# Performance work log

Hardware: AMD Instinct MI355X
Metric: run time of the kernel (lower is better)

Reference implementation:

```python
import jax, jax.numpy as jnp
import numpy as np

T, B, L, F, H = 32, 32, 128, 512, 1024
SCALE = 1.0 / np.sqrt(float(L))  # 1/sqrt(max_demonstration_length)


def _lstm_step(h, c, x, W_ih, W_hh, b_ih, b_hh):
    # PyTorch LSTM gate order: i, f, g, o
    gates = x @ W_ih.T + b_ih + h @ W_hh.T + b_hh
    i, f, g, o = jnp.split(gates, 4, axis=-1)
    c = jax.nn.sigmoid(f) * c + jax.nn.sigmoid(i) * jnp.tanh(g)
    h = jax.nn.sigmoid(o) * jnp.tanh(c)
    return h, c


def setup_inputs() -> dict:
    key = jax.random.key(0)
    ks = jax.random.split(key, 20)
    s = 0.02
    d = {
        'demonstration': jax.random.normal(ks[0], (T, B, L, F), jnp.float32),
        'demonstration_lengths': jax.random.randint(ks[1], (B,), 0, L),
        'current_obs': jax.random.normal(ks[2], (T, B, F), jnp.float32),
        'h0': jnp.zeros((1, B, H), jnp.float32),
        'c0': jnp.zeros((1, B, H), jnp.float32),
        # demonstration_encoder LSTM(F -> H)
        'enc_W_ih': jax.random.normal(ks[3], (4 * H, F), jnp.float32) * s,
        'enc_W_hh': jax.random.normal(ks[4], (4 * H, H), jnp.float32) * s,
        'enc_b_ih': jnp.zeros((4 * H,), jnp.float32),
        'enc_b_hh': jnp.zeros((4 * H,), jnp.float32),
        # attn Linear(H -> H)
        'attn_W': jax.random.normal(ks[5], (H, H), jnp.float32) * s,
        'attn_b': jnp.zeros((H,), jnp.float32),
        # attn_combine MLP: (F + H) -> 4H -> H
        'mlp_W1': jax.random.normal(ks[6], (4 * H, F + H), jnp.float32) * s,
        'mlp_b1': jnp.zeros((4 * H,), jnp.float32),
        'mlp_W2': jax.random.normal(ks[7], (H, 4 * H), jnp.float32) * s,
        'mlp_b2': jnp.zeros((H,), jnp.float32),
        # recurrent LSTM(H -> H)
        'lstm_W_ih': jax.random.normal(ks[8], (4 * H, H), jnp.float32) * s,
        'lstm_W_hh': jax.random.normal(ks[9], (4 * H, H), jnp.float32) * s,
        'lstm_b_ih': jnp.zeros((4 * H,), jnp.float32),
        'lstm_b_hh': jnp.zeros((4 * H,), jnp.float32),
    }
    return d


def reference(demonstration, demonstration_lengths, current_obs, h0, c0,
              enc_W_ih, enc_W_hh, enc_b_ih, enc_b_hh,
              attn_W, attn_b, mlp_W1, mlp_b1, mlp_W2, mlp_b2,
              lstm_W_ih, lstm_W_hh, lstm_b_ih, lstm_b_hh):
    # Encode demonstration[0] (B, L, F) with an LSTM over the L axis.
    x_demo = jnp.transpose(demonstration[0], (1, 0, 2))  # (L, B, F)

    def enc(carry, xt):
        h, c = carry
        h, c = _lstm_step(h, c, xt, enc_W_ih, enc_W_hh, enc_b_ih, enc_b_hh)
        return (h, c), h

    z0 = jnp.zeros((B, H), demonstration.dtype)
    _, demo_enc = jax.lax.scan(enc, (z0, z0), x_demo)  # (L, B, H)
    demo_enc = jnp.transpose(demo_enc, (1, 0, 2))       # (B, L, H)

    # attn(demo_enc) is t-invariant; hoist it out of the loop (same math).
    attn_proj = demo_enc @ attn_W.T + attn_b            # (B, L, H)

    mask = (jnp.arange(L)[None, :] < demonstration_lengths[:, None])
    mask = mask.at[:, 0].set(True)                      # (B, L)

    def step(carry, obs_t):
        h, c = carry  # (B, H)
        scores = jnp.einsum('blh,bh->bl', attn_proj, h) * SCALE
        scores = jnp.where(mask, scores, -jnp.inf)
        w = jax.nn.softmax(scores, axis=-1)             # (B, L)
        ctx = jnp.einsum('bl,blh->bh', w, demo_enc)     # (B, H)
        z = jnp.concatenate([ctx, obs_t], axis=-1)      # (B, H+F)
        m = jax.nn.relu(z @ mlp_W1.T + mlp_b1)          # MLP hidden relu
        x = jax.nn.relu(m @ mlp_W2.T + mlp_b2)          # outer relu in forward
        h, c = _lstm_step(h, c, x, lstm_W_ih, lstm_W_hh, lstm_b_ih, lstm_b_hh)
        return (h, c), h

    (hT, cT), q = jax.lax.scan(step, (h0[0], c0[0]), current_obs)
    return q, hT[None], cT[None]
```

## Files before the change

kernel.cpp:

```cpp
#include <hip/hip_runtime.h>

typedef unsigned short u16;
typedef unsigned int   u32;
typedef short s8v __attribute__((ext_vector_type(8)));
typedef float f4v __attribute__((ext_vector_type(4)));

#define TT 32
#define BB 32
#define LL 128
#define FF 512
#define HH 1024
#define G4 4096
#define SCALE_ 0.08838834764831845f

__device__ __forceinline__ u16 f2bf(float f){
  u32 u = __float_as_uint(f);
  u32 r = u + 0x7fffu + ((u >> 16) & 1u);
  return (u16)(r >> 16);
}
__device__ __forceinline__ float bf2f(u16 s){ return __uint_as_float(((u32)s) << 16); }
__device__ __forceinline__ float sigf(float x){ return 1.f / (1.f + __expf(-x)); }

__device__ __forceinline__ void mfma16(f4v& d, s8v a, s8v b){
  asm("v_mfma_f32_16x16x32_bf16 %0, %1, %2, %0" : "+v"(d) : "v"(a), "v"(b));
}

typedef __attribute__((address_space(3))) u32 as3u32;
typedef __attribute__((address_space(1))) u32 as1u32;
__device__ __forceinline__ void glds16(const u16* g, u16* l){
  __builtin_amdgcn_global_load_lds((const as1u32*)g, (as3u32*)l, 16, 0, 0);
}

__device__ __forceinline__ void stcc_u16(u16* p, u16 v){
  u32 vv = v;
  asm volatile("global_store_short %0, %1, off sc0 sc1" :: "v"(p), "v"(vv) : "memory");
}
__device__ __forceinline__ void stcc_f32(float* p, float v){
  asm volatile("global_store_dword %0, %1, off sc0 sc1" :: "v"(p), "v"(v) : "memory");
}
__device__ __forceinline__ u32 poll_ld(const u32* p){
  u32 v;
  asm volatile("global_load_dword %0, %1, off sc0 sc1\n\ts_waitcnt vmcnt(0)"
               : "=v"(v) : "v"(p) : "memory");
  return v;
}

__device__ __forceinline__ void gbar(u32* cnt, u32 nblk, u32& epoch){
  asm volatile("s_waitcnt vmcnt(0)" ::: "memory");
  __syncthreads();
  ++epoch;
  if (threadIdx.x == 0){
    atomicAdd(cnt, 1u);
    u32 target = epoch * nblk;
    while (poll_ld(cnt) < target) __builtin_amdgcn_s_sleep(1);
  }
  __syncthreads();
}

__device__ __forceinline__ void stg_issue(const u16* __restrict__ src, s8v* tmp, int rstride){
  const int tid = threadIdx.x;
  const int row = tid >> 5, s0 = tid & 31;
  const u16* p = src + (size_t)row * rstride + s0 * 8;
  #pragma unroll
  for (int i = 0; i < 4; i++) tmp[i] = *(const s8v*)(p + i * 256);
}
__device__ __forceinline__ void stg_commit(const s8v* tmp, u16* lds){
  const int tid = threadIdx.x;
  const int row = tid >> 5, s0 = tid & 31;
  char* base = (char*)lds + (row << 11);
  u32 x = (u32)(row & 15) << 4;
  #pragma unroll
  for (int i = 0; i < 4; i++){
    u32 cb = (u32)(s0 + 32 * i) << 4;
    *(s8v*)(base + (cb ^ x)) = tmp[i];
  }
}
__device__ __forceinline__ s8v ldsA(const u16* lds, int row, int cb){
  return *(const s8v*)((const char*)lds + (row << 11) + (cb ^ ((row & 15) << 4)));
}

__global__ void k_convert(const float* __restrict__ src, u16* __restrict__ dst, int n){
  int i = blockIdx.x * blockDim.x + threadIdx.x;
  int st = gridDim.x * blockDim.x;
  for (; i < n; i += st) dst[i] = f2bf(src[i]);
}
__global__ void k_split_w1(const float* __restrict__ w1, u16* __restrict__ w1c, u16* __restrict__ w1o){
  int i = blockIdx.x * blockDim.x + threadIdx.x;
  int st = gridDim.x * blockDim.x;
  const int n = G4 * (FF + HH);
  for (; i < n; i += st){
    int j = i / 1536, k = i - j * 1536;
    u16 v = f2bf(w1[i]);
    if (k < HH) w1c[j * HH + k] = v;
    else        w1o[j * FF + (k - HH)] = v;
  }
}
__global__ void k_addb(const float* __restrict__ a, const float* __restrict__ b,
                       float* __restrict__ o, int n){
  int i = blockIdx.x * blockDim.x + threadIdx.x;
  int st = gridDim.x * blockDim.x;
  for (; i < n; i += st) o[i] = a[i] + b[i];
}
__global__ void k_demo_t(const float* __restrict__ d, u16* __restrict__ o){
  const int n = LL * BB * FF;
  int i = blockIdx.x * blockDim.x + threadIdx.x;
  int st = gridDim.x * blockDim.x;
  for (; i < n; i += st){
    int f = i & 511;
    int row = i >> 9;
    int l = row >> 5, b = row & 31;
    o[i] = f2bf(d[(size_t)b * (LL * FF) + l * FF + f]);
  }
}

template<int RELU>
__global__ void __launch_bounds__(256) k_gemm_bt(const u16* __restrict__ A, const u16* __restrict__ B,
        const float* __restrict__ bias, u16* __restrict__ C, int M, int N, int K)
{
  __shared__ u16 As[128 * 64];
  __shared__ u16 Bs[128 * 64];
  const int tid = threadIdx.x;
  const int lane = tid & 63, wave = tid >> 6;
  const int m0 = blockIdx.x * 128, n0 = blockIdx.y * 128;
  const int wm = wave >> 1, wn = wave & 1;
  const int lr = lane & 15, lk = (lane >> 4) * 8;
  f4v acc[4][4];
  #pragma unroll
  for (int i = 0; i < 4; i++)
    #pragma unroll
    for (int j = 0; j < 4; j++) acc[i][j] = f4v{0.f, 0.f, 0.f, 0.f};

  for (int kt = 0; kt < K; kt += 64){
    #pragma unroll
    for (int i = 0; i < 4; i++){
      int c = tid + i * 256;
      int row = c >> 3, cc = (c & 7) * 8;
      glds16(A + (size_t)(m0 + row) * K + kt + cc, &As[c * 8]);
      glds16(B + (size_t)(n0 + row) * K + kt + cc, &Bs[c * 8]);
    }
    __syncthreads();
    #pragma unroll
    for (int ks = 0; ks < 2; ++ks){
      int ko = ks * 32 + lk;
      s8v av[4], bv[4];
      #pragma unroll
      for (int m = 0; m < 4; m++) av[m] = *(const s8v*)&As[(wm * 64 + m * 16 + lr) * 64 + ko];
      #pragma unroll
      for (int n = 0; n < 4; n++) bv[n] = *(const s8v*)&Bs[(wn * 64 + n * 16 + lr) * 64 + ko];
      #pragma unroll
      for (int m = 0; m < 4; m++)
        #pragma unroll
        for (int n = 0; n < 4; n++) mfma16(acc[m][n], av[m], bv[n]);
    }
    __syncthreads();
  }
  const int r0 = (lane >> 4) * 4;
  #pragma unroll
  for (int m = 0; m < 4; m++){
    #pragma unroll
    for (int n = 0; n < 4; n++){
      int col = n0 + wn * 64 + n * 16 + lr;
      float bc = bias[col];
      #pragma unroll
      for (int r = 0; r < 4; r++){
        int row = m0 + wm * 64 + m * 16 + r0 + r;
        float v = acc[m][n][r] + bc;
        if (RELU) v = fmaxf(v, 0.f);
        C[(size_t)row * N + col] = f2bf(v);
      }
    }
  }
}

union SMemE { u16 stage[32768]; float gx[16][32][17]; };

__global__ void __launch_bounds__(1024, 4) k_encoder(const u16* __restrict__ Whh, const u16* __restrict__ Xih,
      u16* __restrict__ zslot, u16* __restrict__ denc, u32* bar)
{
  __shared__ SMemE sm;
  const int nb = blockIdx.x, tid = threadIdx.x;
  const int lane = tid & 63, w = tid >> 6;
  const int jc = nb * 16;
  const int lr = lane & 15, lk = (lane >> 4) * 8;
  const int eb = tid >> 4, ejj = tid & 15;
  const int rb = (lane >> 4) * 4;

  if (tid < 512) stcc_u16(&zslot[eb * HH + jc + ejj], 0);
  float cr = 0.f;
  u32 epoch = 0;
  gbar(bar, 64, epoch);

  const int kh = (w & 3) * 256;
  const u16* Wb = Whh + (size_t)((w >> 2) * HH + jc + lr) * HH + kh + lk;
  for (int l = 0; l < LL; ++l){
    const u16* hb = (l == 0) ? zslot : (denc + (size_t)(l - 1) * (BB * HH));
    s8v ht[4];
    stg_issue(hb, ht, HH);
    float xi = 0, xf = 0, xg = 0, xo = 0;
    if (tid < 512){
      const u16* xr = Xih + ((size_t)(l * BB + eb)) * G4 + jc + ejj;
      xi = bf2f(xr[0]); xf = bf2f(xr[1024]); xg = bf2f(xr[2048]); xo = bf2f(xr[3072]);
    }
    stg_commit(ht, sm.stage);
    __syncthreads();
    f4v a0 = {0.f,0.f,0.f,0.f}, a1 = {0.f,0.f,0.f,0.f};
    #pragma unroll
    for (int ks = 0; ks < 8; ++ks){
      int cb = (kh + lk + ks * 32) * 2;
      s8v va0 = ldsA(sm.stage, lr,      cb);
      s8v va1 = ldsA(sm.stage, lr + 16, cb);
      s8v vb  = *(const s8v*)(Wb + ks * 32);
      mfma16(a0, va0, vb);
      mfma16(a1, va1, vb);
    }
    __syncthreads();
    #pragma unroll
    for (int r = 0; r < 4; r++){ sm.gx[w][rb + r][lr] = a0[r]; sm.gx[w][16 + rb + r][lr] = a1[r]; }
    __syncthreads();
    if (tid < 512){
      float gi = sm.gx[0][eb][ejj] + sm.gx[1][eb][ejj] + sm.gx[2][eb][ejj] + sm.gx[3][eb][ejj] + xi;
      float gf = sm.gx[4][eb][ejj] + sm.gx[5][eb][ejj] + sm.gx[6][eb][ejj] + sm.gx[7][eb][ejj] + xf;
      float gg = sm.gx[8][eb][ejj] + sm.gx[9][eb][ejj] + sm.gx[10][eb][ejj] + sm.gx[11][eb][ejj] + xg;
      float go = sm.gx[12][eb][ejj] + sm.gx[13][eb][ejj] + sm.gx[14][eb][ejj] + sm.gx[15][eb][ejj] + xo;
      cr = sigf(gf) * cr + sigf(gi) * tanhf(gg);
      float h = sigf(go) * tanhf(cr);
      stcc_u16(&denc[(size_t)l * (BB * HH) + eb * HH + jc + ejj], f2bf(h));
    }
    gbar(bar, 64, epoch);
  }
}

union SMemD {
  u16 stage[32768];
  float gx[16][32][17];
  struct { float swt[128]; } a;
};

__global__ void __launch_bounds__(1024, 4) k_decoder(
    const u16* __restrict__ aproj, const u16* __restrict__ denc, const u16* __restrict__ obsp,
    const u16* __restrict__ W1c, const u16* __restrict__ W2w, const u16* __restrict__ WihL,
    const u16* __restrict__ WhhL, const float* __restrict__ blstm, const float* __restrict__ b2,
    const float* __restrict__ h0, const float* __restrict__ c0, const int* __restrict__ lens,
    float* __restrict__ hfR, u16* __restrict__ hbR, u16* __restrict__ ctxR,
    u16* __restrict__ mbR, u16* __restrict__ xbR, float* __restrict__ scX,
    float* __restrict__ out, u32* bar)
{
  __shared__ SMemD sm;
  const int nb = blockIdx.x, tid = threadIdx.x;
  const int lane = tid & 63, w = tid >> 6;
  const int jc = nb * 16;
  const int lr = lane & 15, lk = (lane >> 4) * 8;
  const int eb = tid >> 4, ejj = tid & 15;
  const int rb = (lane >> 4) * 4;
  const int ab = nb & 31, ah = nb >> 5;

  float cr = 0.f;
  if (tid < 512){
    float hv = h0[eb * HH + jc + ejj];
    stcc_f32(&hfR[eb * HH + jc + ejj], hv);
    stcc_u16(&hbR[eb * HH + jc + ejj], f2bf(hv));
    cr = c0[eb * HH + jc + ejj];
  }
  u32 epoch = 0;
  gbar(bar, 64, epoch);

  for (int t = 0; t < TT; ++t){
    const u16* ctxS = ctxR + (size_t)t * (BB * HH);
    const u16* mbS  = mbR  + (size_t)t * (BB * G4);
    const u16* xbS  = xbR  + (size_t)t * (BB * HH);
    const u16* hbS  = hbR  + (size_t)t * (BB * HH);
    const float* hfS= hfR  + (size_t)t * (BB * HH);
    float* scT = scX + (size_t)t * (BB * 128) + ab * 128;

    {
      const int len = lens[ab];
      float hr[16];
      const float* hp = hfS + ab * HH + lane * 16;
      #pragma unroll
      for (int i = 0; i < 16; i++) hr[i] = hp[i];
      #pragma unroll
      for (int i = 0; i < 4; ++i){
        int l = ah * 64 + w * 4 + i;
        const u16* ap = aproj + ((size_t)(l * BB + ab)) * HH + lane * 16;
        s8v v0 = *(const s8v*)ap;
        s8v v1 = *(const s8v*)(ap + 8);
        float s = 0.f;
        #pragma unroll
        for (int k = 0; k < 8; k++) s += bf2f((u16)v0[k]) * hr[k];
        #pragma unroll
        for (int k = 0; k < 8; k++) s += bf2f((u16)v1[k]) * hr[8 + k];
        #pragma unroll
        for (int off = 32; off > 0; off >>= 1) s += __shfl_down(s, off);
        if (lane == 0){
          s *= SCALE_;
          if (l >= len && l != 0) s = -__builtin_inff();
          stcc_f32(&scT[l], s);
        }
      }
    }
    gbar(bar, 64, epoch);

    {
      if (w == 0){
        float x0 = scT[lane], x1 = scT[lane + 64];
        float mx = fmaxf(x0, x1);
        #pragma unroll
        for (int off = 32; off > 0; off >>= 1) mx = fmaxf(mx, __shfl_xor(mx, off));
        float e0 = __expf(x0 - mx), e1 = __expf(x1 - mx);
        float smv = e0 + e1;
        #pragma unroll
        for (int off = 32; off > 0; off >>= 1) smv += __shfl_xor(smv, off);
        float inv = 1.f / smv;
        sm.a.swt[lane] = e0 * inv;
        sm.a.swt[lane + 64] = e1 * inv;
      }
      __syncthreads();
      if (tid < 512){
        int col = ah * 512 + tid;
        const u16* dp = denc + (size_t)ab * HH + col;
        float acc = 0.f;
        #pragma unroll 4
        for (int l = 0; l < LL; ++l)
          acc += sm.a.swt[l] * bf2f(dp[(size_t)l * (BB * HH)]);
        stcc_u16((u16*)&ctxS[ab * HH + col], f2bf(acc));
      }
    }
    gbar(bar, 64, epoch);

    {
      s8v ct[4];
      stg_issue(ctxS, ct, HH);
      stg_commit(ct, sm.stage);
      __syncthreads();
      const int col0 = nb * 64 + (w >> 2) * 16;
      const int kh = (w & 3) * 256;
      f4v a0 = {0.f,0.f,0.f,0.f}, a1 = {0.f,0.f,0.f,0.f};
      const u16* Bp = W1c + (size_t)(col0 + lr) * HH + kh + lk;
      #pragma unroll
      for (int ks = 0; ks < 8; ++ks){
        int cb = (kh + lk + ks * 32) * 2;
        s8v va0 = ldsA(sm.stage, lr,      cb);
        s8v va1 = ldsA(sm.stage, lr + 16, cb);
        s8v vb  = *(const s8v*)(Bp + ks * 32);
        mfma16(a0, va0, vb);
        mfma16(a1, va1, vb);
      }
      __syncthreads();
      #pragma unroll
      for (int r = 0; r < 4; r++){ sm.gx[w][rb + r][lr] = a0[r]; sm.gx[w][16 + rb + r][lr] = a1[r]; }
      __syncthreads();
      if (tid < 512){
        #pragma unroll
        for (int cg = 0; cg < 4; ++cg){
          int col = nb * 64 + cg * 16 + ejj;
          float v = sm.gx[4 * cg][eb][ejj] + sm.gx[4 * cg + 1][eb][ejj]
                  + sm.gx[4 * cg + 2][eb][ejj] + sm.gx[4 * cg + 3][eb][ejj]
                  + bf2f(obsp[((size_t)(t * BB + eb)) * G4 + col]);
          stcc_u16((u16*)&mbS[eb * G4 + col], f2bf(fmaxf(v, 0.f)));
        }
      }
    }
    gbar(bar, 64, epoch);

    {
      f4v a0 = {0.f,0.f,0.f,0.f}, a1 = {0.f,0.f,0.f,0.f};
      for (int q = 0; q < 4; ++q){
        s8v ct[4];
        stg_issue(mbS + q * 1024, ct, G4);
        stg_commit(ct, sm.stage);
        __syncthreads();
        const u16* Bp = W2w + (size_t)(jc + lr) * G4 + q * 1024 + w * 64 + lk;
        #pragma unroll
        for (int ks = 0; ks < 2; ++ks){
          int cb = (w * 64 + lk + ks * 32) * 2;
          s8v va0 = ldsA(sm.stage, lr,      cb);
          s8v va1 = ldsA(sm.stage, lr + 16, cb);
          s8v vb  = *(const s8v*)(Bp + ks * 32);
          mfma16(a0, va0, vb);
          mfma16(a1, va1, vb);
        }
        __syncthreads();
      }
      #pragma unroll
      for (int r = 0; r < 4; r++){ sm.gx[w][rb + r][lr] = a0[r]; sm.gx[w][16 + rb + r][lr] = a1[r]; }
      __syncthreads();
      if (tid < 512){
        float v = b2[jc + ejj];
        #pragma unroll
        for (int g = 0; g < 16; ++g) v += sm.gx[g][eb][ejj];
        stcc_u16((u16*)&xbS[eb * HH + jc + ejj], f2bf(fmaxf(v, 0.f)));
      }
    }
    gbar(bar, 64, epoch);

    {
      s8v xt[4], ht[4];
      stg_issue(xbS, xt, HH);
      stg_issue(hbS, ht, HH);
      stg_commit(xt, sm.stage);
      __syncthreads();
      const int kh = (w & 3) * 256;
      f4v a0 = {0.f,0.f,0.f,0.f}, a1 = {0.f,0.f,0.f,0.f};
      const u16* Bx = WihL + (size_t)((w >> 2) * HH + jc + lr) * HH + kh + lk;
      #pragma unroll
      for (int ks = 0; ks < 8; ++ks){
        int cb = (kh + lk + ks * 32) * 2;
        s8v va0 = ldsA(sm.stage, lr,      cb);
        s8v va1 = ldsA(sm.stage, lr + 16, cb);
        s8v vb  = *(const s8v*)(Bx + ks * 32);
        mfma16(a0, va0, vb);
        mfma16(a1, va1, vb);
      }
      __syncthreads();
      stg_commit(ht, sm.stage);
      __syncthreads();
      const u16* Bh = WhhL + (size_t)((w >> 2) * HH + jc + lr) * HH + kh + lk;
      #pragma unroll
      for (int ks = 0; ks < 8; ++ks){
        int cb = (kh + lk + ks * 32) * 2;
        s8v va0 = ldsA(sm.stage, lr,      cb);
        s8v va1 = ldsA(sm.stage, lr + 16, cb);
        s8v vb  = *(const s8v*)(Bh + ks * 32);
        mfma16(a0, va0, vb);
        mfma16(a1, va1, vb);
      }
      __syncthreads();
      #pragma unroll
      for (int r = 0; r < 4; r++){ sm.gx[w][rb + r][lr] = a0[r]; sm.gx[w][16 + rb + r][lr] = a1[r]; }
      __syncthreads();
      if (tid < 512){
        int col = jc + ejj;
        float gi = sm.gx[0][eb][ejj] + sm.gx[1][eb][ejj] + sm.gx[2][eb][ejj] + sm.gx[3][eb][ejj] + blstm[col];
        float gf = sm.gx[4][eb][ejj] + sm.gx[5][eb][ejj] + sm.gx[6][eb][ejj] + sm.gx[7][eb][ejj] + blstm[1024 + col];
        float gg = sm.gx[8][eb][ejj] + sm.gx[9][eb][ejj] + sm.gx[10][eb][ejj] + sm.gx[11][eb][ejj] + blstm[2048 + col];
        float go = sm.gx[12][eb][ejj] + sm.gx[13][eb][ejj] + sm.gx[14][eb][ejj] + sm.gx[15][eb][ejj] + blstm[3072 + col];
        cr = sigf(gf) * cr + sigf(gi) * tanhf(gg);
        float h = sigf(go) * tanhf(cr);
        stcc_f32(&out[(size_t)t * (BB * HH) + eb * HH + col], h);
        stcc_f32(&hfR[(size_t)(t + 1) * (BB * HH) + eb * HH + col], h);
        stcc_u16(&hbR[(size_t)(t + 1) * (BB * HH) + eb * HH + col], f2bf(h));
        if (t == TT - 1){
          stcc_f32(&out[1048576 + eb * HH + col], h);
          stcc_f32(&out[1081344 + eb * HH + col], cr);
        }
      }
    }
    gbar(bar, 64, epoch);
  }
}

static constexpr size_t oWihE = 0;
static constexpr size_t oWhhE = oWihE + 4194304;
static constexpr size_t oAttnW= oWhhE + 8388608;
static constexpr size_t oW1C  = oAttnW+ 2097152;
static constexpr size_t oW1O  = oW1C  + 8388608;
static constexpr size_t oW2   = oW1O  + 4194304;
static constexpr size_t oWihL = oW2   + 8388608;
static constexpr size_t oWhhL = oWihL + 8388608;
static constexpr size_t oBEnc = oWhhL + 8388608;
static constexpr size_t oBL   = oBEnc + 16384;
static constexpr size_t oDemoT= oBL   + 16384;
static constexpr size_t oObsB = oDemoT+ 4194304;
static constexpr size_t oXih  = oObsB + 1048576;
static constexpr size_t oObsP = oXih  + 33554432;
static constexpr size_t oDEnc = oObsP + 8388608;
static constexpr size_t oAPrj = oDEnc + 8388608;
static constexpr size_t oZE   = oAPrj + 8388608;
static constexpr size_t oHFR  = oZE   + 65536;
static constexpr size_t oHBR  = oHFR  + 4325376;
static constexpr size_t oCtxR = oHBR  + 2162688;
static constexpr size_t oMBR  = oCtxR + 2097152;
static constexpr size_t oXBR  = oMBR  + 8388608;
static constexpr size_t oScX  = oXBR  + 2097152;
static constexpr size_t oBar  = oScX  + 524288;

extern "C" void kernel_launch(void* const* d_in, const int* in_sizes, int n_in,
                              void* d_out, int out_size, void* d_ws, size_t ws_size,
                              hipStream_t stream)
{
  const float* demo = (const float*)d_in[0];
  const int*   lens = (const int*)  d_in[1];
  const float* obs  = (const float*)d_in[2];
  const float* h0   = (const float*)d_in[3];
  const float* c0   = (const float*)d_in[4];
  const float* eWih = (const float*)d_in[5];
  const float* eWhh = (const float*)d_in[6];
  const float* eBih = (const float*)d_in[7];
  const float* eBhh = (const float*)d_in[8];
  const float* aW   = (const float*)d_in[9];
  const float* aB   = (const float*)d_in[10];
  const float* W1   = (const float*)d_in[11];
  const float* B1   = (const float*)d_in[12];
  const float* W2   = (const float*)d_in[13];
  const float* B2   = (const float*)d_in[14];
  const float* lWih = (const float*)d_in[15];
  const float* lWhh = (const float*)d_in[16];
  const float* lBih = (const float*)d_in[17];
  const float* lBhh = (const float*)d_in[18];

  char* ws = (char*)d_ws;
  u16*  WihE = (u16*)(ws + oWihE);
  u16*  WhhE = (u16*)(ws + oWhhE);
  u16*  AttnW= (u16*)(ws + oAttnW);
  u16*  W1C  = (u16*)(ws + oW1C);
  u16*  W1O  = (u16*)(ws + oW1O);
  u16*  W2w  = (u16*)(ws + oW2);
  u16*  WihL = (u16*)(ws + oWihL);
  u16*  WhhL = (u16*)(ws + oWhhL);
  float* BEnc= (float*)(ws + oBEnc);
  float* BL  = (float*)(ws + oBL);
  u16*  DemoT= (u16*)(ws + oDemoT);
  u16*  ObsB = (u16*)(ws + oObsB);
  u16*  Xih  = (u16*)(ws + oXih);
  u16*  ObsP = (u16*)(ws + oObsP);
  u16*  DEnc = (u16*)(ws + oDEnc);
  u16*  APrj = (u16*)(ws + oAPrj);
  u16*  ZE   = (u16*)(ws + oZE);
  float* HFR = (float*)(ws + oHFR);
  u16*  HBR  = (u16*)(ws + oHBR);
  u16*  CtxR = (u16*)(ws + oCtxR);
  u16*  MBR  = (u16*)(ws + oMBR);
  u16*  XBR  = (u16*)(ws + oXBR);
  float* ScX = (float*)(ws + oScX);
  u32*  Bar  = (u32*)(ws + oBar);

  k_convert<<<1024, 256, 0, stream>>>(eWih, WihE, G4 * FF);
  k_convert<<<1024, 256, 0, stream>>>(eWhh, WhhE, G4 * HH);
  k_convert<<<512,  256, 0, stream>>>(aW,   AttnW, HH * HH);
  k_split_w1<<<1024, 256, 0, stream>>>(W1, W1C, W1O);
  k_convert<<<1024, 256, 0, stream>>>(W2,   W2w,  HH * G4);
  k_convert<<<1024, 256, 0, stream>>>(lWih, WihL, G4 * HH);
  k_convert<<<1024, 256, 0, stream>>>(lWhh, WhhL, G4 * HH);
  k_addb<<<16, 256, 0, stream>>>(eBih, eBhh, BEnc, G4);
  k_addb<<<16, 256, 0, stream>>>(lBih, lBhh, BL, G4);
  k_demo_t<<<1024, 256, 0, stream>>>(demo, DemoT);
  k_convert<<<512, 256, 0, stream>>>(obs, ObsB, TT * BB * FF);
  hipMemsetAsync(Bar, 0, 256, stream);

  {
    dim3 g(LL * BB / 128, G4 / 128);
    k_gemm_bt<0><<<g, 256, 0, stream>>>(DemoT, WihE, BEnc, Xih, LL * BB, G4, FF);
  }
  {
    dim3 g(TT * BB / 128, G4 / 128);
    k_gemm_bt<0><<<g, 256, 0, stream>>>(ObsB, W1O, B1, ObsP, TT * BB, G4, FF);
  }

  k_encoder<<<64, 1024, 0, stream>>>(WhhE, Xih, ZE, DEnc, Bar);

  {
    dim3 g(LL * BB / 128, HH / 128);
    k_gemm_bt<0><<<g, 256, 0, stream>>>(DEnc, AttnW, aB, APrj, LL * BB, HH, HH);
  }

  k_decoder<<<64, 1024, 0, stream>>>(APrj, DEnc, ObsP, W1C, W2w, WihL, WhhL,
                                     BL, B2, h0, c0, lens,
                                     HFR, HBR, CtxR, MBR, XBR, ScX,
                                     (float*)d_out, Bar + 16);
}
```

Baseline: 2.676 ms.

## Split decoder across 128 blocks of 512 threads with batch-half partitioning

The persistent decoder kernel is relaunched with 128 blocks of 512 threads instead of 64 blocks of 1024. The work in each phase is repartitioned: attention scores take quarter-L slices, the MLP1 output columns are halved per block, and the W2 and LSTM GEMMs split the batch into halves so each block handles 16 rows. The aim is to spread the sequential per-step work over more CUs and shorten each phase. The cost is a grid barrier across twice as many blocks, which makes each barrier more expensive. The LDS union is padded to 96KB, which enforces one block per CU.

```diff
diff --git a/kernel.cpp b/kernel.cpp
--- a/kernel.cpp
+++ b/kernel.cpp
@@ -65,6 +65,42 @@
   for (int i = 0; i < 4; i++) tmp[i] = *(const s8v*)(p + i * 256);
 }
 __device__ __forceinline__ void stg_commit(const s8v* tmp, u16* lds){
+  const int tid = threadIdx.x;
+  const int row = tid >> 5, s0 = tid & 31;
+  char* base = (char*)lds + (row << 11);
+  u32 x = (u32)(row & 15) << 4;
+  #pragma unroll
+  for (int i = 0; i < 4; i++){
+    u32 cb = (u32)(s0 + 32 * i) << 4;
+    *(s8v*)(base + (cb ^ x)) = tmp[i];
+  }
+}
+__device__ __forceinline__ void st5_issue(const u16* __restrict__ src, s8v* tmp, int rstride){
+  const int tid = threadIdx.x;
+  const int row = tid >> 4, s0 = tid & 15;
+  const u16* p = src + (size_t)row * rstride + s0 * 8;
+  #pragma unroll
+  for (int i = 0; i < 8; i++) tmp[i] = *(const s8v*)(p + i * 128);
+}
+__device__ __forceinline__ void st5_commit(const s8v* tmp, u16* lds){
+  const int tid = threadIdx.x;
+  const int row = tid >> 4, s0 = tid & 15;
+  char* base = (char*)lds + (row << 11);
+  u32 x = (u32)(row & 15) << 4;
+  #pragma unroll
+  for (int i = 0; i < 8; i++){
+    u32 cb = (u32)(s0 + 16 * i) << 4;
+    *(s8v*)(base + (cb ^ x)) = tmp[i];
+  }
+}
+__device__ __forceinline__ void st16_issue(const u16* __restrict__ src, s8v* tmp, int rstride){
+  const int tid = threadIdx.x;
+  const int row = tid >> 5, s0 = tid & 31;
+  const u16* p = src + (size_t)row * rstride + s0 * 8;
+  #pragma unroll
+  for (int i = 0; i < 4; i++) tmp[i] = *(const s8v*)(p + i * 256);
+}
+__device__ __forceinline__ void st16_commit(const s8v* tmp, u16* lds){
   const int tid = threadIdx.x;
   const int row = tid >> 5, s0 = tid & 31;
   char* base = (char*)lds + (row << 11);
@@ -232,11 +268,12 @@
 
 union SMemD {
   u16 stage[32768];
-  float gx[16][32][17];
+  float gx[8][32][17];
   struct { float swt[128]; } a;
+  char pad[98304];
 };
 
-__global__ void __launch_bounds__(1024, 4) k_decoder(
+__global__ void __launch_bounds__(512, 1) k_decoder(
     const u16* __restrict__ aproj, const u16* __restrict__ denc, const u16* __restrict__ obsp,
     const u16* __restrict__ W1c, const u16* __restrict__ W2w, const u16* __restrict__ WihL,
     const u16* __restrict__ WhhL, const float* __restrict__ blstm, const float* __restrict__ b2,
@@ -248,21 +285,23 @@
   __shared__ SMemD sm;
   const int nb = blockIdx.x, tid = threadIdx.x;
   const int lane = tid & 63, w = tid >> 6;
-  const int jc = nb * 16;
   const int lr = lane & 15, lk = (lane >> 4) * 8;
+  const int rb = (lane >> 4) * 4;
   const int eb = tid >> 4, ejj = tid & 15;
-  const int rb = (lane >> 4) * 4;
-  const int ab = nb & 31, ah = nb >> 5;
+  const int ab = nb & 31, aq = nb >> 5;
+  const int pb = nb >> 1, bh = nb & 1;
+  const int jc = pb * 16;
 
   float cr = 0.f;
-  if (tid < 512){
-    float hv = h0[eb * HH + jc + ejj];
-    stcc_f32(&hfR[eb * HH + jc + ejj], hv);
-    stcc_u16(&hbR[eb * HH + jc + ejj], f2bf(hv));
-    cr = c0[eb * HH + jc + ejj];
+  if (tid < 256){
+    int b = bh * 16 + (tid >> 4), col = jc + (tid & 15);
+    float hv = h0[b * HH + col];
+    stcc_f32(&hfR[b * HH + col], hv);
+    stcc_u16(&hbR[b * HH + col], f2bf(hv));
+    cr = c0[b * HH + col];
   }
   u32 epoch = 0;
-  gbar(bar, 64, epoch);
+  gbar(bar, 128, epoch);
 
   for (int t = 0; t < TT; ++t){
     const u16* ctxS = ctxR + (size_t)t * (BB * HH);
@@ -280,7 +319,7 @@
       for (int i = 0; i < 16; i++) hr[i] = hp[i];
       #pragma unroll
       for (int i = 0; i < 4; ++i){
-        int l = ah * 64 + w * 4 + i;
+        int l = aq * 32 + w * 4 + i;
         const u16* ap = aproj + ((size_t)(l * BB + ab)) * HH + lane * 16;
         s8v v0 = *(const s8v*)ap;
         s8v v1 = *(const s8v*)(ap + 8);
@@ -298,7 +337,7 @@
         }
       }
     }
-    gbar(bar, 64, epoch);
+    gbar(bar, 128, epoch);
 
     {
       if (w == 0){
@@ -315,8 +354,8 @@
         sm.a.swt[lane + 64] = e1 * inv;
       }
       __syncthreads();
-      if (tid < 512){
-        int col = ah * 512 + tid;
+      if (tid < 256){
+        int col = aq * 256 + tid;
         const u16* dp = denc + (size_t)ab * HH + col;
         float acc = 0.f;
         #pragma unroll 4
@@ -325,14 +364,14 @@
         stcc_u16((u16*)&ctxS[ab * HH + col], f2bf(acc));
       }
     }
-    gbar(bar, 64, epoch);
+    gbar(bar, 128, epoch);
 
     {
-      s8v ct[4];
-      stg_issue(ctxS, ct, HH);
-      stg_commit(ct, sm.stage);
-      __syncthreads();
-      const int col0 = nb * 64 + (w >> 2) * 16;
+      s8v ct[8];
+      st5_issue(ctxS, ct, HH);
+      st5_commit(ct, sm.stage);
+      __syncthreads();
+      const int col0 = nb * 32 + (w >> 2) * 16;
       const int kh = (w & 3) * 256;
       f4v a0 = {0.f,0.f,0.f,0.f}, a1 = {0.f,0.f,0.f,0.f};
       const u16* Bp = W1c + (size_t)(col0 + lr) * HH + kh + lk;
@@ -349,103 +388,91 @@
       #pragma unroll
       for (int r = 0; r < 4; r++){ sm.gx[w][rb + r][lr] = a0[r]; sm.gx[w][16 + rb + r][lr] = a1[r]; }
       __syncthreads();
-      if (tid < 512){
-        #pragma unroll
-        for (int cg = 0; cg < 4; ++cg){
-          int col = nb * 64 + cg * 16 + ejj;
-          float v = sm.gx[4 * cg][eb][ejj] + sm.gx[4 * cg + 1][eb][ejj]
-                  + sm.gx[4 * cg + 2][eb][ejj] + sm.gx[4 * cg + 3][eb][ejj]
-                  + bf2f(obsp[((size_t)(t * BB + eb)) * G4 + col]);
-          stcc_u16((u16*)&mbS[eb * G4 + col], f2bf(fmaxf(v, 0.f)));
-        }
-      }
-    }
-    gbar(bar, 64, epoch);
+      #pragma unroll
+      for (int cg = 0; cg < 2; ++cg){
+        int col = nb * 32 + cg * 16 + ejj;
+        float v = sm.gx[4 * cg][eb][ejj] + sm.gx[4 * cg + 1][eb][ejj]
+                + sm.gx[4 * cg + 2][eb][ejj] + sm.gx[4 * cg + 3][eb][ejj]
+                + bf2f(obsp[((size_t)(t * BB + eb)) * G4 + col]);
+        stcc_u16((u16*)&mbS[eb * G4 + col], f2bf(fmaxf(v, 0.f)));
+      }
+    }
+    gbar(bar, 128, epoch);
 
     {
-      f4v a0 = {0.f,0.f,0.f,0.f}, a1 = {0.f,0.f,0.f,0.f};
+      f4v a0 = {0.f,0.f,0.f,0.f};
       for (int q = 0; q < 4; ++q){
         s8v ct[4];
-        stg_issue(mbS + q * 1024, ct, G4);
-        stg_commit(ct, sm.stage);
+        st16_issue(mbS + (size_t)(bh * 16) * G4 + q * 1024, ct, G4);
+        st16_commit(ct, sm.stage);
         __syncthreads();
-        const u16* Bp = W2w + (size_t)(jc + lr) * G4 + q * 1024 + w * 64 + lk;
-        #pragma unroll
-        for (int ks = 0; ks < 2; ++ks){
-          int cb = (w * 64 + lk + ks * 32) * 2;
-          s8v va0 = ldsA(sm.stage, lr,      cb);
-          s8v va1 = ldsA(sm.stage, lr + 16, cb);
+        const u16* Bp = W2w + (size_t)(jc + lr) * G4 + q * 1024 + w * 128 + lk;
+        #pragma unroll
+        for (int ks = 0; ks < 4; ++ks){
+          int cb = (w * 128 + lk + ks * 32) * 2;
+          s8v va0 = ldsA(sm.stage, lr, cb);
           s8v vb  = *(const s8v*)(Bp + ks * 32);
           mfma16(a0, va0, vb);
-          mfma16(a1, va1, vb);
         }
         __syncthreads();
       }
       #pragma unroll
-      for (int r = 0; r < 4; r++){ sm.gx[w][rb + r][lr] = a0[r]; sm.gx[w][16 + rb + r][lr] = a1[r]; }
-      __syncthreads();
-      if (tid < 512){
-        float v = b2[jc + ejj];
-        #pragma unroll
-        for (int g = 0; g < 16; ++g) v += sm.gx[g][eb][ejj];
-        stcc_u16((u16*)&xbS[eb * HH + jc + ejj], f2bf(fmaxf(v, 0.f)));
-      }
-    }
-    gbar(bar, 64, epoch);
+      for (int r = 0; r < 4; r++) sm.gx[w][rb + r][lr] = a0[r];
+      __syncthreads();
+      if (tid < 256){
+        int bb = tid >> 4, cc = tid & 15;
+        float v = b2[jc + cc];
+        #pragma unroll
+        for (int g = 0; g < 8; ++g) v += sm.gx[g][bb][cc];
+        stcc_u16((u16*)&xbS[(bh * 16 + bb) * HH + jc + cc], f2bf(fmaxf(v, 0.f)));
+      }
+    }
+    gbar(bar, 128, epoch);
 
     {
       s8v xt[4], ht[4];
-      stg_issue(xbS, xt, HH);
-      stg_issue(hbS, ht, HH);
-      stg_commit(xt, sm.stage);
-      __syncthreads();
-      const int kh = (w & 3) * 256;
-      f4v a0 = {0.f,0.f,0.f,0.f}, a1 = {0.f,0.f,0.f,0.f};
-      const u16* Bx = WihL + (size_t)((w >> 2) * HH + jc + lr) * HH + kh + lk;
-      #pragma unroll
-      for (int ks = 0; ks < 8; ++ks){
+      st16_issue(xbS + (size_t)(bh * 16) * HH, xt, HH);
+      st16_issue(hbS + (size_t)(bh * 16) * HH, ht, HH);
+      st16_commit(xt, sm.stage);
+      st16_commit(ht, sm.stage + 16384);
+      __syncthreads();
+      const int gate = w >> 1, kh = (w & 1) * 512;
+      f4v a0 = {0.f,0.f,0.f,0.f};
+      const u16* Bx = WihL + (size_t)(gate * HH + jc + lr) * HH + kh + lk;
+      #pragma unroll
+      for (int ks = 0; ks < 16; ++ks){
         int cb = (kh + lk + ks * 32) * 2;
-        s8v va0 = ldsA(sm.stage, lr,      cb);
-        s8v va1 = ldsA(sm.stage, lr + 16, cb);
-        s8v vb  = *(const s8v*)(Bx + ks * 32);
-        mfma16(a0, va0, vb);
-        mfma16(a1, va1, vb);
-      }
-      __syncthreads();
-      stg_commit(ht, sm.stage);
-      __syncthreads();
-      const u16* Bh = WhhL + (size_t)((w >> 2) * HH + jc + lr) * HH + kh + lk;
-      #pragma unroll
-      for (int ks = 0; ks < 8; ++ks){
+        mfma16(a0, ldsA(sm.stage, lr, cb), *(const s8v*)(Bx + ks * 32));
+      }
+      const u16* Bh = WhhL + (size_t)(gate * HH + jc + lr) * HH + kh + lk;
+      #pragma unroll
+      for (int ks = 0; ks < 16; ++ks){
         int cb = (kh + lk + ks * 32) * 2;
-        s8v va0 = ldsA(sm.stage, lr,      cb);
-        s8v va1 = ldsA(sm.stage, lr + 16, cb);
-        s8v vb  = *(const s8v*)(Bh + ks * 32);
-        mfma16(a0, va0, vb);
-        mfma16(a1, va1, vb);
-      }
-      __syncthreads();
-      #pragma unroll
-      for (int r = 0; r < 4; r++){ sm.gx[w][rb + r][lr] = a0[r]; sm.gx[w][16 + rb + r][lr] = a1[r]; }
-      __syncthreads();
-      if (tid < 512){
-        int col = jc + ejj;
-        float gi = sm.gx[0][eb][ejj] + sm.gx[1][eb][ejj] + sm.gx[2][eb][ejj] + sm.gx[3][eb][ejj] + blstm[col];
-        float gf = sm.gx[4][eb][ejj] + sm.gx[5][eb][ejj] + sm.gx[6][eb][ejj] + sm.gx[7][eb][ejj] + blstm[1024 + col];
-        float gg = sm.gx[8][eb][ejj] + sm.gx[9][eb][ejj] + sm.gx[10][eb][ejj] + sm.gx[11][eb][ejj] + blstm[2048 + col];
-        float go = sm.gx[12][eb][ejj] + sm.gx[13][eb][ejj] + sm.gx[14][eb][ejj] + sm.gx[15][eb][ejj] + blstm[3072 + col];
+        mfma16(a0, ldsA(sm.stage + 16384, lr, cb), *(const s8v*)(Bh + ks * 32));
+      }
+      __syncthreads();
+      #pragma unroll
+      for (int r = 0; r < 4; r++) sm.gx[w][rb + r][lr] = a0[r];
+      __syncthreads();
+      if (tid < 256){
+        int bb = tid >> 4, cc = tid & 15;
+        int b = bh * 16 + bb, col = jc + cc;
+        float gi = sm.gx[0][bb][cc] + sm.gx[1][bb][cc] + blstm[col];
+        float gf = sm.gx[2][bb][cc] + sm.gx[3][bb][cc] + blstm[1024 + col];
+        float gg = sm.gx[4][bb][cc] + sm.gx[5][bb][cc] + blstm[2048 + col];
+        float go = sm.gx[6][bb][cc] + sm.gx[7][bb][cc] + blstm[3072 + col];
         cr = sigf(gf) * cr + sigf(gi) * tanhf(gg);
         float h = sigf(go) * tanhf(cr);
-        stcc_f32(&out[(size_t)t * (BB * HH) + eb * HH + col], h);
-        stcc_f32(&hfR[(size_t)(t + 1) * (BB * HH) + eb * HH + col], h);
-        stcc_u16(&hbR[(size_t)(t + 1) * (BB * HH) + eb * HH + col], f2bf(h));
+        stcc_f32(&out[(size_t)t * (BB * HH) + b * HH + col], h);
+        stcc_f32(&hfR[(size_t)(t + 1) * (BB * HH) + b * HH + col], h);
+        stcc_u16(&hbR[(size_t)(t + 1) * (BB * HH) + b * HH + col], f2bf(h));
         if (t == TT - 1){
-          stcc_f32(&out[1048576 + eb * HH + col], h);
-          stcc_f32(&out[1081344 + eb * HH + col], cr);
+          stcc_f32(&out[1048576 + b * HH + col], h);
+          stcc_f32(&out[1081344 + b * HH + col], cr);
         }
       }
     }
-    gbar(bar, 64, epoch);
+    gbar(bar, 128, epoch);
   }
 }
 
@@ -553,7 +580,7 @@
     k_gemm_bt<0><<<g, 256, 0, stream>>>(DEnc, AttnW, aB, APrj, LL * BB, HH, HH);
   }
 
-  k_decoder<<<64, 1024, 0, stream>>>(APrj, DEnc, ObsP, W1C, W2w, WihL, WhhL,
+  k_decoder<<<128, 512, 0, stream>>>(APrj, DEnc, ObsP, W1C, W2w, WihL, WhhL,
                                      BL, B2, h0, c0, lens,
                                      HFR, HBR, CtxR, MBR, XBR, ScX,
                                      (float*)d_out, Bar + 16);
```

After: 2.663 ms. Within noise of the previous version (-0.5%).
